# Performance work log

Hardware: AMD Instinct MI355X
Metric: run time of the kernel (lower is better)

Reference implementation:

```python
import jax, jax.numpy as jnp
import numpy as np

DIM = 768
NUM_HEADS = 12
HEAD_DIM = DIM // NUM_HEADS
SCALE = HEAD_DIM ** -0.5
B, N = 16, 640  # N = 8*8 + 24*24


def setup_inputs() -> dict:
    key = jax.random.key(0)
    ks = jax.random.split(key, 4)
    x = jax.random.normal(ks[0], (B, N, DIM), dtype=jnp.float32)
    # weights stored input-major: y = x @ W + b (equiv. to torch Linear with W = weight.T)
    qkv_w = jax.random.normal(ks[1], (DIM, 3 * DIM), dtype=jnp.float32) * (DIM ** -0.5)
    qkv_b = jnp.zeros((3 * DIM,), dtype=jnp.float32)
    proj_w = jax.random.normal(ks[2], (DIM, DIM), dtype=jnp.float32) * (DIM ** -0.5)
    proj_b = jnp.zeros((DIM,), dtype=jnp.float32)
    w = jnp.ones((2,), dtype=jnp.float32)
    return {"x": x, "qkv_w": qkv_w, "qkv_b": qkv_b, "proj_w": proj_w,
            "proj_b": proj_b, "w": w, "t_h": 8, "t_w": 8, "s_h": 24, "s_w": 24}


def reference(x, qkv_w, qkv_b, proj_w, proj_b, w, t_h, t_w, s_h, s_w):
    b, n, c = x.shape
    qkv = (x @ qkv_w + qkv_b).reshape(b, n, 3, NUM_HEADS, HEAD_DIM)
    qkv = jnp.transpose(qkv, (2, 0, 3, 1, 4))  # [3, B, H, N, D]
    q, k, v = qkv[0], qkv[1], qkv[2]
    attn = jnp.einsum('bhnd,bhmd->bhnm', q, k) * SCALE  # [B,H,N,N]
    attn0 = jax.nn.softmax(attn, axis=-1)
    attn1 = jnp.square(jax.nn.relu(attn))
    ws = jax.nn.softmax(w)  # exp(w_i)/sum(exp(w)) blend weights
    attn = attn0 * ws[0] + attn1 * ws[1]
    out = jnp.einsum('bhnm,bhmd->bhnd', attn, v)  # [B,H,N,D]
    out = jnp.transpose(out, (0, 2, 1, 3)).reshape(b, n, c)
    return out @ proj_w + proj_b
```

## Files before the change

### kernel.cpp

```cpp
#include <hip/hip_runtime.h>
#include <hip/hip_bf16.h>

typedef __attribute__((ext_vector_type(8))) short short8;
typedef __attribute__((ext_vector_type(4))) float floatx4;
typedef __hip_bfloat16 bf16;

#define DIM 768
#define NH 12
#define HD 64
#define BB 16
#define NN 640
#define BH (BB*NH)
#define MROWS (BB*NN)
#define QKVN (3*DIM)
#define SCALE 0.125f

__device__ __forceinline__ floatx4 mfma16(short8 a, short8 b, floatx4 c) {
    return __builtin_amdgcn_mfma_f32_16x16x32_bf16(a, b, c, 0, 0, 0);
}

__device__ __forceinline__ void async_ld16(const bf16* g, bf16* l) {
    __builtin_amdgcn_global_load_lds(
        (const __attribute__((address_space(1))) void*)g,
        (__attribute__((address_space(3))) void*)l, 16, 0, 0);
}

__device__ __forceinline__ unsigned pack_bf2(float a, float b) {
    union { bf16 h; unsigned short u; } x, y;
    x.h = __float2bfloat16(a); y.h = __float2bfloat16(b);
    return (unsigned)x.u | ((unsigned)y.u << 16);
}


__global__ void cvt_x(const float* __restrict__ x, bf16* __restrict__ xb, int n4) {
    int i = blockIdx.x * blockDim.x + threadIdx.x;
    if (i >= n4) return;
    float4 v = ((const float4*)x)[i];
    bf16* p = xb + (size_t)i * 4;
    p[0] = __float2bfloat16(v.x);
    p[1] = __float2bfloat16(v.y);
    p[2] = __float2bfloat16(v.z);
    p[3] = __float2bfloat16(v.w);
}

__global__ void tr_cvt(const float* __restrict__ src, bf16* __restrict__ dst, int R, int C) {
    __shared__ float tile[32][33];
    int bx = blockIdx.x, by = blockIdx.y;
    int tx = threadIdx.x, ty = threadIdx.y;
    for (int j = 0; j < 4; ++j)
        tile[ty + j*8][tx] = src[(size_t)(by*32 + ty + j*8) * C + bx*32 + tx];
    __syncthreads();
    for (int j = 0; j < 4; ++j)
        dst[(size_t)(bx*32 + ty + j*8) * R + by*32 + tx] = __float2bfloat16(tile[tx][ty + j*8]);
}

__global__ void v_tr(const bf16* __restrict__ qkv, bf16* __restrict__ vT) {
    __shared__ bf16 tile[32][33];
    int bhc = blockIdx.z;
    int b = bhc / NH, h = bhc - b * NH;
    int tt = blockIdx.x, dt = blockIdx.y;
    int tx = threadIdx.x, ty = threadIdx.y;
    for (int j = 0; j < 4; ++j) {
        int tok = tt*32 + ty + j*8;
        tile[ty + j*8][tx] = qkv[(size_t)(b*NN + tok)*QKVN + 2*DIM + h*HD + dt*32 + tx];
    }
    __syncthreads();
    for (int j = 0; j < 4; ++j) {
        int d = dt*32 + ty + j*8;
        vT[((size_t)bhc*HD + d)*NN + tt*32 + tx] = tile[tx][ty + j*8];
    }
}

template<int MODE>
__global__ __launch_bounds__(256) void gemm_bt(
    const bf16* __restrict__ A, const bf16* __restrict__ B, const float* __restrict__ bias,
    int M, int N, int K,
    bf16* __restrict__ outb, float* __restrict__ outf)
{
    __shared__ __align__(16) bf16 As[128*32];
    __shared__ __align__(16) bf16 Bs[128*32];

    const int t = threadIdx.x;
    const int lane = t & 63, wave = t >> 6;
    const int l15 = lane & 15, quad = lane >> 4;
    const int wm = (wave >> 1) * 64, wn = (wave & 1) * 64;
    const int m0 = blockIdx.x * 128, n0 = blockIdx.y * 128;

    floatx4 acc[4][4];
    floatx4 zero = {0.f, 0.f, 0.f, 0.f};
    for (int i = 0; i < 4; ++i)
        for (int j = 0; j < 4; ++j)
            acc[i][j] = zero;

    for (int kk = 0; kk < K; kk += 32) {
        __syncthreads();
        for (int s = 0; s < 2; ++s) {
            int cid = s * 256 + t;
            int row = cid >> 2;
            int c8  = (cid & 3) << 3;
            int lbase = (s * 256 + wave * 64) * 8;
            async_ld16(A + (size_t)(m0 + row) * K + kk + c8, As + lbase);
            async_ld16(B + (size_t)(n0 + row) * K + kk + c8, Bs + lbase);
        }
        __syncthreads();
        short8 af[4], bfv[4];
        for (int fm = 0; fm < 4; ++fm)
            af[fm] = *(const short8*)(As + (wm + fm*16 + l15) * 32 + quad * 8);
        for (int fn = 0; fn < 4; ++fn)
            bfv[fn] = *(const short8*)(Bs + (wn + fn*16 + l15) * 32 + quad * 8);
        for (int fm = 0; fm < 4; ++fm)
            for (int fn = 0; fn < 4; ++fn)
                acc[fm][fn] = mfma16(af[fm], bfv[fn], acc[fm][fn]);
    }

    for (int fm = 0; fm < 4; ++fm) {
        for (int fn = 0; fn < 4; ++fn) {
            int n = n0 + wn + fn*16 + l15;
            float bn = bias[n];
            for (int r = 0; r < 4; ++r) {
                int m = m0 + wm + fm*16 + quad*4 + r;
                float v = acc[fm][fn][r] + bn;
                if (MODE == 0) {
                    if (n < DIM) v *= SCALE;
                    outb[(size_t)m * N + n] = __float2bfloat16(v);
                } else {
                    outf[(size_t)m * N + n] = v;
                }
            }
        }
    }
}

__global__ __launch_bounds__(256) void attn_kernel(
    const bf16* __restrict__ qkv, const bf16* __restrict__ vT,
    const float* __restrict__ w2, bf16* __restrict__ ao)
{
    const int bh = blockIdx.x;
    const int b = bh / NH, h = bh - b * NH;
    const int t = threadIdx.x;
    const int wave = t >> 6;
    const int lane = t & 63;
    const int l15 = lane & 15, quad = lane >> 4;
    const int qrow0 = blockIdx.y * 64 + wave * 16;

    float w0 = w2[0], w1 = w2[1];
    float wmx = fmaxf(w0, w1);
    float e0 = __expf(w0 - wmx), e1 = __expf(w1 - wmx);
    float ws0 = e0 / (e0 + e1), ws1 = 1.0f - ws0;

    __shared__ __align__(16) bf16 Kb[2][32*64];
    __shared__ __align__(16) bf16 Vb[2][64*32];
    __shared__ __align__(16) bf16 Ps[4][16*40];
    __shared__ __align__(16) bf16 Pr[4][16*40];

    const bf16* kg = qkv + (size_t)(b*NN)*QKVN + DIM + h*HD;
    const bf16* vg = vT + (size_t)bh * HD * NN;

    const bf16* qrow = qkv + (size_t)(b*NN + qrow0 + l15) * QKVN + h*HD;
    short8 aq0 = *(const short8*)(qrow + quad*8);
    short8 aq1 = *(const short8*)(qrow + 32 + quad*8);

    const int krow = t >> 3;
    const int kcg  = ((t & 7) ^ (krow & 7)) * 8;
    const int vrow = t >> 2;
    const int vcg  = ((t & 3) ^ ((t >> 3) & 3)) * 8;

    const bf16* kgp = kg + (size_t)krow * QKVN + kcg;
    const bf16* vgp = vg + (size_t)vrow * NN + vcg;

    async_ld16(kgp, &Kb[0][wave*512]);
    async_ld16(vgp, &Vb[0][wave*512]);

    floatx4 zero = {0.f, 0.f, 0.f, 0.f};
    floatx4 accS[4], accR[4];
    for (int i = 0; i < 4; ++i) { accS[i] = zero; accR[i] = zero; }
    float lsum = 0.f;

    const int chLo = (quad ^ (l15 & 7)) * 8;
    const int chHi = chLo ^ 32;
    const int vslotbase = ((l15 >> 1) & 3);

    unsigned* PsW = (unsigned*)&Ps[wave][0];
    unsigned* PrW = (unsigned*)&Pr[wave][0];
    const int wb = l15*20 + quad*2;
    const bf16* PsR = &Ps[wave][l15*40 + quad*8];
    const bf16* PrR = &Pr[wave][l15*40 + quad*8];

    for (int kt = 0; kt < 20; ++kt) {
        const int cur = kt & 1;
        __syncthreads();
        if (kt + 1 < 20) {
            kgp += 32 * QKVN;
            vgp += 32;
            async_ld16(kgp, &Kb[cur^1][wave*512]);
            async_ld16(vgp, &Vb[cur^1][wave*512]);
        }

        const bf16* Kc = Kb[cur];
        short8 ak0lo = *(const short8*)(Kc + l15*64 + chLo);
        short8 ak0hi = *(const short8*)(Kc + l15*64 + chHi);
        short8 ak1lo = *(const short8*)(Kc + (16 + l15)*64 + chLo);
        short8 ak1hi = *(const short8*)(Kc + (16 + l15)*64 + chHi);

        const bf16* Vc = Vb[cur];
        short8 bv[4];
        for (int dt = 0; dt < 4; ++dt)
            bv[dt] = *(const short8*)(Vc + (dt*16 + l15)*32 + (quad ^ vslotbase)*8);

        floatx4 s0 = zero, s1 = zero;
        s0 = mfma16(ak0lo, aq0, s0);
        s0 = mfma16(ak0hi, aq1, s0);
        s1 = mfma16(ak1lo, aq0, s1);
        s1 = mfma16(ak1hi, aq1, s1);

        float ex0[4], ex1[4], rq0[4], rq1[4];
        for (int r = 0; r < 4; ++r) {
            ex0[r] = __expf(s0[r]);
            ex1[r] = __expf(s1[r]);
            float m0 = fmaxf(s0[r], 0.f), m1 = fmaxf(s1[r], 0.f);
            rq0[r] = m0 * m0;
            rq1[r] = m1 * m1;
            lsum += ex0[r] + ex1[r];
        }

        PsW[wb]     = pack_bf2(ex0[0], ex0[1]);
        PsW[wb + 1] = pack_bf2(ex0[2], ex0[3]);
        PsW[wb + 8] = pack_bf2(ex1[0], ex1[1]);
        PsW[wb + 9] = pack_bf2(ex1[2], ex1[3]);
        PrW[wb]     = pack_bf2(rq0[0], rq0[1]);
        PrW[wb + 1] = pack_bf2(rq0[2], rq0[3]);
        PrW[wb + 8] = pack_bf2(rq1[0], rq1[1]);
        PrW[wb + 9] = pack_bf2(rq1[2], rq1[3]);

        short8 paS = *(const short8*)PsR;
        short8 paR = *(const short8*)PrR;

        for (int dt = 0; dt < 4; ++dt) {
            accS[dt] = mfma16(paS, bv[dt], accS[dt]);
            accR[dt] = mfma16(paR, bv[dt], accR[dt]);
        }
    }

    lsum += __shfl_xor(lsum, 16);
    lsum += __shfl_xor(lsum, 32);
    float invq[4];
    for (int r = 0; r < 4; ++r)
        invq[r] = 1.0f / __shfl(lsum, quad*4 + r);

    for (int dt = 0; dt < 4; ++dt) {
        for (int r = 0; r < 4; ++r) {
            float v = ws0 * accS[dt][r] * invq[r] + ws1 * accR[dt][r];
            int tok = qrow0 + quad*4 + r;
            ao[((size_t)(b * NN + tok)) * DIM + h * HD + dt*16 + l15] = __float2bfloat16(v);
        }
    }
}


extern "C" void kernel_launch(void* const* d_in, const int* in_sizes, int n_in,
                              void* d_out, int out_size, void* d_ws, size_t ws_size,
                              hipStream_t stream) {
    const float* x      = (const float*)d_in[0];
    const float* qkv_w  = (const float*)d_in[1];
    const float* qkv_b  = (const float*)d_in[2];
    const float* proj_w = (const float*)d_in[3];
    const float* proj_b = (const float*)d_in[4];
    const float* w2     = (const float*)d_in[5];
    float* out = (float*)d_out;

    bf16* xb   = (bf16*)d_ws;
    bf16* qwT  = xb   + (size_t)MROWS * DIM;
    bf16* pwT  = qwT  + (size_t)QKVN * DIM;
    bf16* qkvb = pwT  + (size_t)DIM * DIM;
    bf16* vT   = qkvb + (size_t)MROWS * QKVN;
    bf16* ao   = xb;

    cvt_x<<<(MROWS * DIM / 4 + 255) / 256, 256, 0, stream>>>(x, xb, MROWS * DIM / 4);
    tr_cvt<<<dim3(QKVN / 32, DIM / 32), dim3(32, 8), 0, stream>>>(qkv_w, qwT, DIM, QKVN);
    tr_cvt<<<dim3(DIM / 32, DIM / 32), dim3(32, 8), 0, stream>>>(proj_w, pwT, DIM, DIM);

    gemm_bt<0><<<dim3(MROWS / 128, QKVN / 128), 256, 0, stream>>>(
        xb, qwT, qkv_b, MROWS, QKVN, DIM, qkvb, nullptr);

    v_tr<<<dim3(NN / 32, HD / 32, BH), dim3(32, 8), 0, stream>>>(qkvb, vT);

    attn_kernel<<<dim3(BH, NN / 64), 256, 0, stream>>>(qkvb, vT, w2, ao);

    gemm_bt<1><<<dim3(MROWS / 128, DIM / 128), 256, 0, stream>>>(
        ao, pwT, proj_b, MROWS, DIM, DIM, nullptr, out);
}
```

Baseline: 248.6 us.

## Use exp2 with folded log2e scale, truncating bf16 packing, and swapped GEMM grid

Q is now pre-scaled by SCALE*log2(e), so the attention kernel can use the native exp2 instruction. The relu-squared branch is corrected by multiplying its blend weight by ln2^2. The float-to-bf16 RNE packing is replaced with a single byte-permute truncation, and LDS writes are merged into 64-bit stores. The GEMM grids are also transposed so consecutive blocks share the same A row tile for better L2 reuse, and the attention loop is unrolled by 2. Truncating instead of rounding adds a small bias in the P values.

```diff
diff --git a/kernel.cpp b/kernel.cpp
--- a/kernel.cpp
+++ b/kernel.cpp
@@ -14,6 +14,8 @@
 #define MROWS (BB*NN)
 #define QKVN (3*DIM)
 #define SCALE 0.125f
+#define QSCALE 0.18033688011113205f
+#define LN2SQ 0.4804530139182014f
 
 __device__ __forceinline__ floatx4 mfma16(short8 a, short8 b, floatx4 c) {
     return __builtin_amdgcn_mfma_f32_16x16x32_bf16(a, b, c, 0, 0, 0);
@@ -25,10 +27,16 @@
         (__attribute__((address_space(3))) void*)l, 16, 0, 0);
 }
 
-__device__ __forceinline__ unsigned pack_bf2(float a, float b) {
-    union { bf16 h; unsigned short u; } x, y;
-    x.h = __float2bfloat16(a); y.h = __float2bfloat16(b);
-    return (unsigned)x.u | ((unsigned)y.u << 16);
+__device__ __forceinline__ unsigned pack_trunc(float a, float b) {
+    return __builtin_amdgcn_perm(__float_as_uint(b), __float_as_uint(a), 0x07060302u);
+}
+
+__device__ __forceinline__ float fexp2(float x) {
+#if __has_builtin(__builtin_amdgcn_exp2f)
+    return __builtin_amdgcn_exp2f(x);
+#else
+    return exp2f(x);
+#endif
 }
 
 
@@ -84,7 +92,7 @@
     const int lane = t & 63, wave = t >> 6;
     const int l15 = lane & 15, quad = lane >> 4;
     const int wm = (wave >> 1) * 64, wn = (wave & 1) * 64;
-    const int m0 = blockIdx.x * 128, n0 = blockIdx.y * 128;
+    const int m0 = blockIdx.y * 128, n0 = blockIdx.x * 128;
 
     floatx4 acc[4][4];
     floatx4 zero = {0.f, 0.f, 0.f, 0.f};
@@ -121,7 +129,7 @@
                 int m = m0 + wm + fm*16 + quad*4 + r;
                 float v = acc[fm][fn][r] + bn;
                 if (MODE == 0) {
-                    if (n < DIM) v *= SCALE;
+                    if (n < DIM) v *= QSCALE;
                     outb[(size_t)m * N + n] = __float2bfloat16(v);
                 } else {
                     outf[(size_t)m * N + n] = v;
@@ -146,7 +154,8 @@
     float w0 = w2[0], w1 = w2[1];
     float wmx = fmaxf(w0, w1);
     float e0 = __expf(w0 - wmx), e1 = __expf(w1 - wmx);
-    float ws0 = e0 / (e0 + e1), ws1 = 1.0f - ws0;
+    float ws0 = e0 / (e0 + e1);
+    float ws1 = (1.0f - ws0) * LN2SQ;
 
     __shared__ __align__(16) bf16 Kb[2][32*64];
     __shared__ __align__(16) bf16 Vb[2][64*32];
@@ -186,6 +195,7 @@
     const bf16* PsR = &Ps[wave][l15*40 + quad*8];
     const bf16* PrR = &Pr[wave][l15*40 + quad*8];
 
+#pragma unroll 2
     for (int kt = 0; kt < 20; ++kt) {
         const int cur = kt & 1;
         __syncthreads();
@@ -215,22 +225,18 @@
 
         float ex0[4], ex1[4], rq0[4], rq1[4];
         for (int r = 0; r < 4; ++r) {
-            ex0[r] = __expf(s0[r]);
-            ex1[r] = __expf(s1[r]);
+            ex0[r] = fexp2(s0[r]);
+            ex1[r] = fexp2(s1[r]);
             float m0 = fmaxf(s0[r], 0.f), m1 = fmaxf(s1[r], 0.f);
             rq0[r] = m0 * m0;
             rq1[r] = m1 * m1;
             lsum += ex0[r] + ex1[r];
         }
 
-        PsW[wb]     = pack_bf2(ex0[0], ex0[1]);
-        PsW[wb + 1] = pack_bf2(ex0[2], ex0[3]);
-        PsW[wb + 8] = pack_bf2(ex1[0], ex1[1]);
-        PsW[wb + 9] = pack_bf2(ex1[2], ex1[3]);
-        PrW[wb]     = pack_bf2(rq0[0], rq0[1]);
-        PrW[wb + 1] = pack_bf2(rq0[2], rq0[3]);
-        PrW[wb + 8] = pack_bf2(rq1[0], rq1[1]);
-        PrW[wb + 9] = pack_bf2(rq1[2], rq1[3]);
+        *(uint2*)(PsW + wb)     = make_uint2(pack_trunc(ex0[0], ex0[1]), pack_trunc(ex0[2], ex0[3]));
+        *(uint2*)(PsW + wb + 8) = make_uint2(pack_trunc(ex1[0], ex1[1]), pack_trunc(ex1[2], ex1[3]));
+        *(uint2*)(PrW + wb)     = make_uint2(pack_trunc(rq0[0], rq0[1]), pack_trunc(rq0[2], rq0[3]));
+        *(uint2*)(PrW + wb + 8) = make_uint2(pack_trunc(rq1[0], rq1[1]), pack_trunc(rq1[2], rq1[3]));
 
         short8 paS = *(const short8*)PsR;
         short8 paR = *(const short8*)PrR;
@@ -279,13 +285,13 @@
     tr_cvt<<<dim3(QKVN / 32, DIM / 32), dim3(32, 8), 0, stream>>>(qkv_w, qwT, DIM, QKVN);
     tr_cvt<<<dim3(DIM / 32, DIM / 32), dim3(32, 8), 0, stream>>>(proj_w, pwT, DIM, DIM);
 
-    gemm_bt<0><<<dim3(MROWS / 128, QKVN / 128), 256, 0, stream>>>(
+    gemm_bt<0><<<dim3(QKVN / 128, MROWS / 128), 256, 0, stream>>>(
         xb, qwT, qkv_b, MROWS, QKVN, DIM, qkvb, nullptr);
 
     v_tr<<<dim3(NN / 32, HD / 32, BH), dim3(32, 8), 0, stream>>>(qkvb, vT);
 
     attn_kernel<<<dim3(BH, NN / 64), 256, 0, stream>>>(qkvb, vT, w2, ao);
 
-    gemm_bt<1><<<dim3(MROWS / 128, DIM / 128), 256, 0, stream>>>(
+    gemm_bt<1><<<dim3(DIM / 128, MROWS / 128), 256, 0, stream>>>(
         ao, pwT, proj_b, MROWS, DIM, DIM, nullptr, out);
 }
```

After: 247.4 us. No clear change (-0.5%).
